# Optimization experiments

Hardware: AMD Instinct MI355X
Metric: run time of the kernel (lower is better)

The kernel has to match this reference:

```python
import jax, jax.numpy as jnp
import numpy as np


def _safe_sqrt(x):
    # cdist-style euclidean distance with grad-safe sqrt at 0
    return jnp.sqrt(jnp.maximum(x, 1e-12))


def setup_inputs() -> dict:
    key = jax.random.key(0)
    k1, k2, k3 = jax.random.split(key, 3)
    B, P, D, C, N = 256, 196, 768, 15, 12544
    return {
        "query_features": jax.random.normal(k1, (B, P, D), dtype=jnp.float32),
        "keys": jax.random.normal(k2, (C, P, D), dtype=jnp.float32),
        "embeddings": jax.random.normal(k3, (N, D), dtype=jnp.float32),
        "num_samples": 196,
    }


def _retrieve_key(query_features, keys):
    # torch.cdist(new_flat.unsqueeze(1), keys_flat.unsqueeze(0)).squeeze(1); min over classes
    B = query_features.shape[0]
    C = keys.shape[0]
    q = query_features.reshape(B, -1)  # [B, P*D]
    k = keys.reshape(C, -1)            # [C, P*D]
    sq = (jnp.sum(q * q, axis=1)[:, None]
          + jnp.sum(k * k, axis=1)[None, :]
          - 2.0 * (q @ k.T))           # [B, C] squared distances via GEMM
    d = _safe_sqrt(sq)
    min_dist = jnp.min(d, axis=1)
    min_idx = jnp.argmin(d, axis=1)
    return min_dist, min_idx


def _fps(embeddings, num_samples):
    # furthest_point_sampling_embeddings: iterative cdist-to-last-centroid,
    # running min of distances, argmax picks next centroid.
    # (torch version seeds with a random index; we use index 0 deterministically)
    N = embeddings.shape[0]
    sqn = jnp.sum(embeddings * embeddings, axis=1)  # [N]

    def step(carry, _):
        dists, last = carry
        c = embeddings[last]                          # [D]
        cur = _safe_sqrt(sqn - 2.0 * (embeddings @ c) + jnp.sum(c * c))
        dists = jnp.minimum(dists, cur)
        nxt = jnp.argmax(dists).astype(jnp.int32)
        return (dists, nxt), nxt

    init = (jnp.full((N,), jnp.inf, dtype=embeddings.dtype), jnp.int32(0))
    _, idxs = jax.lax.scan(step, init, None, length=num_samples - 1)
    idxs = jnp.concatenate([jnp.zeros((1,), dtype=idxs.dtype), idxs])
    return embeddings[idxs]  # [num_samples, D]


def reference(query_features, keys, embeddings, num_samples):
    min_dist, min_idx = _retrieve_key(query_features, keys)
    samples = _fps(embeddings, num_samples)
    return min_dist, min_idx, samples
```

## Files before the change

### kernel.cpp

```cpp
#include <hip/hip_runtime.h>
#include <math.h>

typedef unsigned long long u64;
typedef unsigned int u32;

#define L_TOT  150528
#define ROW4   37632
#define NCHUNK 7
#define CH4    5376
#define R_ITERS 84
#define NBT    32
#define BTILE  8
#define NCLS   15

#define N_E    12544
#define DIM    768
#define NBLK   256
#define PPB    49
#define NSAMP  196
#define EPB    (PPB*DIM)

__device__ __forceinline__ float wave_sum(float v) {
#pragma unroll
  for (int m = 1; m < 64; m <<= 1) v += __shfl_xor(v, m, 64);
  return v;
}

__device__ __forceinline__ u64 wave_max_u64(u64 v) {
#pragma unroll
  for (int m = 1; m < 64; m <<= 1) {
    u64 o = __shfl_xor(v, m, 64);
    if (o > v) v = o;
  }
  return v;
}

__global__ __launch_bounds__(256) void retrieve_partial(
    const float* __restrict__ q, const float* __restrict__ k,
    float* __restrict__ part, float* __restrict__ kkpart) {
  const int bt = blockIdx.x;
  const int lc = blockIdx.y;
  const int tid = threadIdx.x;
  const int w = tid >> 6, lane = tid & 63;
  const int cbase = w * 4;
  const int ccnt = (w == 3) ? 3 : 4;
  const float4* qf = (const float4*)q;
  const float4* kf = (const float4*)k;
  const int fbase = lc * CH4 + lane;

  float acc[BTILE][4];
  float qq[BTILE];
  float kkv[4];
#pragma unroll
  for (int b = 0; b < BTILE; ++b) {
    qq[b] = 0.f;
#pragma unroll
    for (int c = 0; c < 4; ++c) acc[b][c] = 0.f;
  }
#pragma unroll
  for (int c = 0; c < 4; ++c) kkv[c] = 0.f;

  for (int it = 0; it < R_ITERS; ++it) {
    const int f = fbase + it * 64;
    float4 kv[4];
#pragma unroll
    for (int c = 0; c < 4; ++c)
      if (c < ccnt) kv[c] = kf[(size_t)(cbase + c) * ROW4 + f];
    if (bt == 0) {
#pragma unroll
      for (int c = 0; c < 4; ++c)
        if (c < ccnt)
          kkv[c] += kv[c].x*kv[c].x + kv[c].y*kv[c].y + kv[c].z*kv[c].z + kv[c].w*kv[c].w;
    }
#pragma unroll
    for (int b = 0; b < BTILE; ++b) {
      float4 qv = qf[(size_t)(bt * BTILE + b) * ROW4 + f];
#pragma unroll
      for (int c = 0; c < 4; ++c)
        if (c < ccnt)
          acc[b][c] += qv.x*kv[c].x + qv.y*kv[c].y + qv.z*kv[c].z + qv.w*kv[c].w;
      if (w == 3)
        qq[b] += qv.x*qv.x + qv.y*qv.y + qv.z*qv.z + qv.w*qv.w;
    }
  }

  const size_t pb = (size_t)(lc * NBT + bt) * 16;
#pragma unroll
  for (int b = 0; b < BTILE; ++b) {
#pragma unroll
    for (int c = 0; c < 4; ++c) {
      float v = wave_sum(acc[b][c]);
      if (lane == 0 && c < ccnt) part[(pb + cbase + c) * 8 + b] = v;
    }
    if (w == 3) {
      float v = wave_sum(qq[b]);
      if (lane == 0) part[(pb + 15) * 8 + b] = v;
    }
  }
  if (bt == 0) {
#pragma unroll
    for (int c = 0; c < 4; ++c) {
      float v = wave_sum(kkv[c]);
      if (lane == 0 && c < ccnt) kkpart[lc * 16 + cbase + c] = v;
    }
  }
}

__global__ __launch_bounds__(256) void retrieve_reduce(
    const float* __restrict__ part, const float* __restrict__ kkpart,
    float* __restrict__ out) {
  __shared__ float kn[NCLS];
  const int t = threadIdx.x;
  if (t < NCLS) {
    float s = 0.f;
    for (int lc = 0; lc < NCHUNK; ++lc) s += kkpart[lc * 16 + t];
    kn[t] = s;
  }
  __syncthreads();
  const int bt = t >> 3, bi = t & 7;
  float qq = 0.f;
  for (int lc = 0; lc < NCHUNK; ++lc)
    qq += part[((size_t)(lc * NBT + bt) * 16 + 15) * 8 + bi];
  float dmin = INFINITY;
  int didx = 0;
  for (int c = 0; c < NCLS; ++c) {
    float dot = 0.f;
    for (int lc = 0; lc < NCHUNK; ++lc)
      dot += part[((size_t)(lc * NBT + bt) * 16 + c) * 8 + bi];
    float d2 = qq + kn[c] - 2.f * dot;
    float d = sqrtf(fmaxf(d2, 1e-12f));
    if (d < dmin) { dmin = d; didx = c; }
  }
  out[t] = dmin;
  out[256 + t] = (float)didx;
}

__global__ __launch_bounds__(1024, 4) void fps_kernel(
    const float* __restrict__ emb,
    u64* __restrict__ words,
    u64* __restrict__ result,
    float* __restrict__ out_samples) {
  extern __shared__ float e_lds[];
  const int tid = threadIdx.x;
  const int blk = blockIdx.x;
  const int w = tid >> 6, lane = tid & 63;
  const int q4 = lane >> 4;
  const int r = lane & 15;
  const int pl = w * 4 + q4;
  const bool valid = pl < PPB;
  const int p = valid ? pl : 0;

  __shared__ int hist[NSAMP];
  __shared__ u64 wkey[16];
  __shared__ u64 swin[4];

  {
    const float* src = emb + (size_t)blk * EPB;
    for (int i = tid; i < EPB; i += 1024) e_lds[i] = src[i];
  }
  __syncthreads();

  const float4* ef = (const float4*)(e_lds + (size_t)p * DIM);
  float sq;
  {
    float ss = 0.f;
#pragma unroll
    for (int jj = 0; jj < 12; ++jj) {
      float4 v = ef[r + jj * 16];
      ss = fmaf(v.x, v.x, ss); ss = fmaf(v.y, v.y, ss);
      ss = fmaf(v.z, v.z, ss); ss = fmaf(v.w, v.w, ss);
    }
#pragma unroll
    for (int m = 1; m < 16; m <<= 1) ss += __shfl_xor(ss, m, 64);
    sq = ss;
  }
  float dist2 = INFINITY;
  int last = 0;
  if (tid == 0) hist[0] = 0;
  __syncthreads();

  for (int s = 1; s < NSAMP; ++s) {
    const int buf = (s & 1) * NBLK;

    const float4* cf = (const float4*)(emb + (size_t)last * DIM);
    float4 cv[12];
#pragma unroll
    for (int jj = 0; jj < 12; ++jj) cv[jj] = cf[r + jj * 16];

    float a = 0.f, cn = 0.f;
#pragma unroll
    for (int jj = 0; jj < 12; ++jj) {
      float4 e4 = ef[r + jj * 16];
      float4 c4 = cv[jj];
      a = fmaf(e4.x, c4.x, a); a = fmaf(e4.y, c4.y, a);
      a = fmaf(e4.z, c4.z, a); a = fmaf(e4.w, c4.w, a);
      cn = fmaf(c4.x, c4.x, cn); cn = fmaf(c4.y, c4.y, cn);
      cn = fmaf(c4.z, c4.z, cn); cn = fmaf(c4.w, c4.w, cn);
    }
#pragma unroll
    for (int m = 1; m < 16; m <<= 1) {
      a += __shfl_xor(a, m, 64);
      cn += __shfl_xor(cn, m, 64);
    }

    u64 key = 0ull;
    if (valid) {
      float d2 = sq - 2.f * a + cn;
      if (d2 < dist2) dist2 = d2;
      key = ((u64)__float_as_uint(dist2) << 32) |
            (u32)(~(u32)(blk * PPB + pl));
    }
#pragma unroll
    for (int m = 16; m < 64; m <<= 1) {
      u64 o = __shfl_xor(key, m, 64);
      if (o > key) key = o;
    }
    if (lane == 0) wkey[w] = key;
    __syncthreads();

    if (w == 0) {
      u64 k = wkey[lane & 15];
#pragma unroll
      for (int m = 1; m < 16; m <<= 1) {
        u64 o = __shfl_xor(k, m, 64);
        if (o > k) k = o;
      }
      if (lane == 0) {
        const u32 bidx = ~(u32)(k & 0xffffffffull);
        const u32 bdist = (u32)(k >> 32);
        const u64 word = ((u64)s << 48) | ((u64)bdist << 16) | (u64)bidx;
        __hip_atomic_store(&words[buf + blk], word, __ATOMIC_RELAXED,
                           __HIP_MEMORY_SCOPE_AGENT);
      }
    }

    if (blk == 0) {
      if (tid < NBLK) {
        u64 w64;
        for (;;) {
          w64 = __hip_atomic_load(&words[buf + tid], __ATOMIC_RELAXED,
                                  __HIP_MEMORY_SCOPE_AGENT);
          if ((w64 >> 48) >= (u64)s) break;
        }
        u64 kk = (((w64 >> 16) & 0xffffffffull) << 32) |
                 (u64)(u32)(~(u32)(w64 & 0xffffull));
        kk = wave_max_u64(kk);
        if (lane == 0) swin[w] = kk;
      }
      __syncthreads();
      if (tid == 0) {
        u64 m = swin[0];
#pragma unroll
        for (int qi = 1; qi < 4; ++qi) if (swin[qi] > m) m = swin[qi];
        const int widx = (int)(~(u32)(m & 0xffffffffull));
        hist[s] = widx;
        __hip_atomic_store(&result[s & 1], ((u64)s << 32) | (u32)widx,
                           __ATOMIC_RELAXED, __HIP_MEMORY_SCOPE_AGENT);
      }
      __syncthreads();
    } else {
      if (tid == 0) {
        u64 r0, r1, r2, r3, rr;
        for (;;) {
          r0 = __hip_atomic_load(&result[s & 1], __ATOMIC_RELAXED,
                                 __HIP_MEMORY_SCOPE_AGENT);
          r1 = __hip_atomic_load(&result[s & 1], __ATOMIC_RELAXED,
                                 __HIP_MEMORY_SCOPE_AGENT);
          r2 = __hip_atomic_load(&result[s & 1], __ATOMIC_RELAXED,
                                 __HIP_MEMORY_SCOPE_AGENT);
          r3 = __hip_atomic_load(&result[s & 1], __ATOMIC_RELAXED,
                                 __HIP_MEMORY_SCOPE_AGENT);
          if ((r3 >> 32) >= (u64)s) { rr = r3; break; }
          if ((r2 >> 32) >= (u64)s) { rr = r2; break; }
          if ((r1 >> 32) >= (u64)s) { rr = r1; break; }
          if ((r0 >> 32) >= (u64)s) { rr = r0; break; }
        }
        hist[s] = (int)(u32)(rr & 0xffffffffull);
      }
      __syncthreads();
    }
    last = hist[s];
  }

  if (blk < NSAMP) {
    const int idx = hist[blk];
    const float4* src = (const float4*)(emb + (size_t)idx * DIM);
    float4* dst = (float4*)(out_samples + (size_t)blk * DIM);
    if (tid < DIM / 4) dst[tid] = src[tid];
  }
}

extern "C" void kernel_launch(void* const* d_in, const int* in_sizes, int n_in,
                              void* d_out, int out_size, void* d_ws, size_t ws_size,
                              hipStream_t stream) {
  const float* q   = (const float*)d_in[0];
  const float* k   = (const float*)d_in[1];
  const float* emb = (const float*)d_in[2];
  float* out = (float*)d_out;

  u64* words  = (u64*)d_ws;
  u64* result = (u64*)((char*)d_ws + 4096);
  float* part   = (float*)((char*)d_ws + 8192);
  float* kkpart = part + 28672;

  hipMemsetAsync(d_ws, 0, 4096 + 16, stream);

  hipLaunchKernelGGL(retrieve_partial, dim3(NBT, NCHUNK), dim3(256), 0, stream,
                     q, k, part, kkpart);
  hipLaunchKernelGGL(retrieve_reduce, dim3(1), dim3(256), 0, stream,
                     part, kkpart, out);

  hipFuncSetAttribute((const void*)fps_kernel,
                      hipFuncAttributeMaxDynamicSharedMemorySize,
                      EPB * sizeof(float));

  float* samples = out + 512;
  void* args[] = {(void*)&emb, (void*)&words, (void*)&result, (void*)&samples};
  hipLaunchCooperativeKernel((void*)fps_kernel, dim3(NBLK), dim3(1024), args,
                             EPB * sizeof(float), stream);
}
```

Before: 902.5 us.

## Replace two-hop FPS reduction with all-block redundant argmax over padded slots

```diff
diff --git a/kernel.cpp b/kernel.cpp
--- a/kernel.cpp
+++ b/kernel.cpp
@@ -19,19 +19,11 @@
 #define PPB    49
 #define NSAMP  196
 #define EPB    (PPB*DIM)
+#define WSTRIDE 16
 
 __device__ __forceinline__ float wave_sum(float v) {
 #pragma unroll
   for (int m = 1; m < 64; m <<= 1) v += __shfl_xor(v, m, 64);
-  return v;
-}
-
-__device__ __forceinline__ u64 wave_max_u64(u64 v) {
-#pragma unroll
-  for (int m = 1; m < 64; m <<= 1) {
-    u64 o = __shfl_xor(v, m, 64);
-    if (o > v) v = o;
-  }
   return v;
 }
 
@@ -138,7 +130,6 @@
 __global__ __launch_bounds__(1024, 4) void fps_kernel(
     const float* __restrict__ emb,
     u64* __restrict__ words,
-    u64* __restrict__ result,
     float* __restrict__ out_samples) {
   extern __shared__ float e_lds[];
   const int tid = threadIdx.x;
@@ -229,56 +220,36 @@
         const u32 bidx = ~(u32)(k & 0xffffffffull);
         const u32 bdist = (u32)(k >> 32);
         const u64 word = ((u64)s << 48) | ((u64)bdist << 16) | (u64)bidx;
-        __hip_atomic_store(&words[buf + blk], word, __ATOMIC_RELAXED,
-                           __HIP_MEMORY_SCOPE_AGENT);
-      }
-    }
-
-    if (blk == 0) {
-      if (tid < NBLK) {
-        u64 w64;
-        for (;;) {
-          w64 = __hip_atomic_load(&words[buf + tid], __ATOMIC_RELAXED,
-                                  __HIP_MEMORY_SCOPE_AGENT);
-          if ((w64 >> 48) >= (u64)s) break;
-        }
-        u64 kk = (((w64 >> 16) & 0xffffffffull) << 32) |
-                 (u64)(u32)(~(u32)(w64 & 0xffffull));
-        kk = wave_max_u64(kk);
-        if (lane == 0) swin[w] = kk;
-      }
-      __syncthreads();
-      if (tid == 0) {
-        u64 m = swin[0];
-#pragma unroll
-        for (int qi = 1; qi < 4; ++qi) if (swin[qi] > m) m = swin[qi];
-        const int widx = (int)(~(u32)(m & 0xffffffffull));
-        hist[s] = widx;
-        __hip_atomic_store(&result[s & 1], ((u64)s << 32) | (u32)widx,
+        __hip_atomic_store(&words[(size_t)(buf + blk) * WSTRIDE], word,
                            __ATOMIC_RELAXED, __HIP_MEMORY_SCOPE_AGENT);
       }
-      __syncthreads();
-    } else {
-      if (tid == 0) {
-        u64 r0, r1, r2, r3, rr;
-        for (;;) {
-          r0 = __hip_atomic_load(&result[s & 1], __ATOMIC_RELAXED,
-                                 __HIP_MEMORY_SCOPE_AGENT);
-          r1 = __hip_atomic_load(&result[s & 1], __ATOMIC_RELAXED,
-                                 __HIP_MEMORY_SCOPE_AGENT);
-          r2 = __hip_atomic_load(&result[s & 1], __ATOMIC_RELAXED,
-                                 __HIP_MEMORY_SCOPE_AGENT);
-          r3 = __hip_atomic_load(&result[s & 1], __ATOMIC_RELAXED,
-                                 __HIP_MEMORY_SCOPE_AGENT);
-          if ((r3 >> 32) >= (u64)s) { rr = r3; break; }
-          if ((r2 >> 32) >= (u64)s) { rr = r2; break; }
-          if ((r1 >> 32) >= (u64)s) { rr = r1; break; }
-          if ((r0 >> 32) >= (u64)s) { rr = r0; break; }
-        }
-        hist[s] = (int)(u32)(rr & 0xffffffffull);
-      }
-      __syncthreads();
-    }
+    }
+
+    if (tid < NBLK) {
+      u64 w64;
+      const u64* slot = &words[(size_t)(buf + tid) * WSTRIDE];
+      for (;;) {
+        w64 = __hip_atomic_load(slot, __ATOMIC_RELAXED,
+                                __HIP_MEMORY_SCOPE_AGENT);
+        if ((w64 >> 48) >= (u64)s) break;
+      }
+      u64 kk = (((w64 >> 16) & 0xffffffffull) << 32) |
+               (u64)(u32)(~(u32)(w64 & 0xffffull));
+#pragma unroll
+      for (int m = 1; m < 64; m <<= 1) {
+        u64 o = __shfl_xor(kk, m, 64);
+        if (o > kk) kk = o;
+      }
+      if (lane == 0) swin[w] = kk;
+    }
+    __syncthreads();
+    if (tid == 0) {
+      u64 m = swin[0];
+#pragma unroll
+      for (int qi = 1; qi < 4; ++qi) if (swin[qi] > m) m = swin[qi];
+      hist[s] = (int)(~(u32)(m & 0xffffffffull));
+    }
+    __syncthreads();
     last = hist[s];
   }
 
@@ -298,12 +269,11 @@
   const float* emb = (const float*)d_in[2];
   float* out = (float*)d_out;
 
-  u64* words  = (u64*)d_ws;
-  u64* result = (u64*)((char*)d_ws + 4096);
-  float* part   = (float*)((char*)d_ws + 8192);
+  u64* words = (u64*)d_ws;
+  float* part   = (float*)((char*)d_ws + 65536);
   float* kkpart = part + 28672;
 
-  hipMemsetAsync(d_ws, 0, 4096 + 16, stream);
+  hipMemsetAsync(words, 0, 2 * NBLK * WSTRIDE * sizeof(u64), stream);
 
   hipLaunchKernelGGL(retrieve_partial, dim3(NBT, NCHUNK), dim3(256), 0, stream,
                      q, k, part, kkpart);
@@ -315,7 +285,7 @@
                       EPB * sizeof(float));
 
   float* samples = out + 512;
-  void* args[] = {(void*)&emb, (void*)&words, (void*)&result, (void*)&samples};
+  void* args[] = {(void*)&emb, (void*)&words, (void*)&samples};
   hipLaunchCooperativeKernel((void*)fps_kernel, dim3(NBLK), dim3(1024), args,
                              EPB * sizeof(float), stream);
 }
```

After: 907.9 us. About the same (+0.6%).
